# Kernel tuning notes

Hardware: AMD Instinct MI355X
Metric: run time of the kernel (lower is better)

## Reference

```python
import jax, jax.numpy as jnp
import numpy as np

B, H, W, C = 4, 64, 64, 512
G = 32  # GroupNorm groups
EPS = 1e-6


def setup_inputs() -> dict:
    key = jax.random.key(0)
    ks = jax.random.split(key, 9)
    s = C ** -0.5
    return {
        "x": jax.random.normal(ks[0], (B, H, W, C), dtype=jnp.float32),
        "gn_scale": jnp.ones((C,), dtype=jnp.float32),
        "gn_bias": jnp.zeros((C,), dtype=jnp.float32),
        "wq": jax.random.normal(ks[1], (C, C), dtype=jnp.float32) * s,
        "bq": jnp.zeros((C,), dtype=jnp.float32),
        "wk": jax.random.normal(ks[2], (C, C), dtype=jnp.float32) * s,
        "bk": jnp.zeros((C,), dtype=jnp.float32),
        "wv": jax.random.normal(ks[3], (C, C), dtype=jnp.float32) * s,
        "bv": jnp.zeros((C,), dtype=jnp.float32),
        "wo": jax.random.normal(ks[4], (C, C), dtype=jnp.float32) * s,
        "bo": jnp.zeros((C,), dtype=jnp.float32),
    }


def reference(x, gn_scale, gn_bias, wq, bq, wk, bk, wv, bv, wo, bo):
    b, h, w, c = x.shape
    # GroupNorm(32, eps=1e-6): normalize over (H, W, channels-within-group)
    xg = x.reshape(b, h, w, G, c // G)
    mean = xg.mean(axis=(1, 2, 4), keepdims=True)
    var = xg.var(axis=(1, 2, 4), keepdims=True)
    hn = ((xg - mean) * jax.lax.rsqrt(var + EPS)).reshape(b, h, w, c)
    hn = hn * gn_scale + gn_bias
    # 1x1 convs == per-pixel matmuls
    n = h * w
    hf = hn.reshape(b, n, c)
    q = hf @ wq + bq  # [b, n, c]
    k = hf @ wk + bk
    v = hf @ wv + bv
    # attention with materialized scores (faithful to source math)
    scores = jnp.einsum('bqc,bkc->bqk', q, k) * (c ** -0.5)
    attn = jax.nn.softmax(scores, axis=2)
    o = jnp.einsum('bkc,bqk->bqc', v, attn)  # [b, n, c]
    o = o @ wo + bo
    return o.reshape(b, h, w, c) + x
```

## Files before the change

### kernel.cpp

```cpp
#include <hip/hip_runtime.h>
#include <stdint.h>

typedef unsigned short u16;
typedef __bf16 bf16x8 __attribute__((ext_vector_type(8)));
typedef float f32x4 __attribute__((ext_vector_type(4)));
typedef uint32_t u32x2 __attribute__((ext_vector_type(2)));
typedef uint32_t u32x4 __attribute__((ext_vector_type(4)));

#define NB 4
#define NC 512
#define NG 32
#define NSEQ 4096
#define NM (NB*NSEQ)

#define MFMA_(a,b,c) __builtin_amdgcn_mfma_f32_16x16x32_bf16(a,b,c,0,0,0)
#define SWZ(rl) (((((rl) ^ ((rl)>>2)) & 7)) << 4)

__device__ __forceinline__ u16 f2bf(float f){
  uint32_t u = __builtin_bit_cast(uint32_t, f);
  u += 0x7FFFu + ((u >> 16) & 1u);
  return (u16)(u >> 16);
}
__device__ __forceinline__ float bfu(uint32_t lo16){
  return __builtin_bit_cast(float, lo16 << 16);
}
__device__ __forceinline__ uint32_t pk2(float a, float b){
  return (uint32_t)f2bf(a) | ((uint32_t)f2bf(b) << 16);
}

__device__ __forceinline__ void gll16(const void* g, void* l){
  __builtin_amdgcn_global_load_lds(
      (const __attribute__((address_space(1))) void*)g,
      (__attribute__((address_space(3))) void*)l, 16, 0, 0);
}

__global__ void k_zero(float* p, int n){
  int i = blockIdx.x*blockDim.x + threadIdx.x;
  if (i < n) p[i] = 0.f;
}

__global__ __launch_bounds__(256) void k_gn_stats(const float* __restrict__ x, float* __restrict__ stats){
  int blk = blockIdx.x;
  int ch = blk & 7, bg = blk >> 3;
  int g = bg & (NG-1), b = bg >> 5;
  int t = threadIdx.x;
  const float* base = x + (size_t)b*NSEQ*NC + g*16 + (t&3)*4;
  float s1 = 0.f, s2 = 0.f;
  for (int p = ch*512 + (t>>2); p < (ch+1)*512; p += 64){
    float4 v = *(const float4*)(base + (size_t)p*NC);
    s1 += v.x+v.y+v.z+v.w;
    s2 += v.x*v.x + v.y*v.y + v.z*v.z + v.w*v.w;
  }
  #pragma unroll
  for (int o = 32; o; o >>= 1){ s1 += __shfl_xor(s1, o); s2 += __shfl_xor(s2, o); }
  __shared__ float a1[4], a2[4];
  if ((t & 63) == 0){ a1[t>>6] = s1; a2[t>>6] = s2; }
  __syncthreads();
  if (t == 0){
    atomicAdd(&stats[bg*2+0], a1[0]+a1[1]+a1[2]+a1[3]);
    atomicAdd(&stats[bg*2+1], a2[0]+a2[1]+a2[2]+a2[3]);
  }
}

__global__ __launch_bounds__(256) void k_gn_apply(const float* __restrict__ x, const float* __restrict__ stats,
    const float* __restrict__ gsc, const float* __restrict__ gbi, u16* __restrict__ hn){
  const float inv_cnt = 1.f/((float)NSEQ*16.f);
  size_t total = (size_t)NM*NC/4;
  for (size_t i = (size_t)blockIdx.x*blockDim.x + threadIdx.x; i < total; i += (size_t)gridDim.x*blockDim.x){
    size_t flat = i*4;
    int c = (int)(flat & (NC-1));
    int b = (int)(flat >> 21);
    int g = c >> 4;
    float s1 = stats[(b*NG+g)*2], s2 = stats[(b*NG+g)*2+1];
    float mean = s1*inv_cnt;
    float rstd = rsqrtf(s2*inv_cnt - mean*mean + 1e-6f);
    float4 v = *(const float4*)(x + flat);
    float4 sc = *(const float4*)(gsc + c);
    float4 bi = *(const float4*)(gbi + c);
    ushort4 o;
    o.x = f2bf((v.x-mean)*rstd*sc.x + bi.x);
    o.y = f2bf((v.y-mean)*rstd*sc.y + bi.y);
    o.z = f2bf((v.z-mean)*rstd*sc.z + bi.z);
    o.w = f2bf((v.w-mean)*rstd*sc.w + bi.w);
    *(ushort4*)(hn + flat) = o;
  }
}

__global__ __launch_bounds__(256) void k_wtrans4(const float* __restrict__ wq, const float* __restrict__ wk,
    const float* __restrict__ wv, const float* __restrict__ wo,
    u16* __restrict__ wqkvT, u16* __restrict__ woT){
  int j = blockIdx.x*256 + threadIdx.x;
  int wsel = j >> 18, r = j & 262143;
  int n = r >> 9, k = r & 511;
  const float* src = wsel==0?wq : wsel==1?wk : wsel==2?wv : wo;
  u16 v = f2bf(src[k*512 + n]);
  if (wsel < 3) wqkvT[(size_t)wsel*262144 + r] = v;
  else          woT[r] = v;
}

__global__ __launch_bounds__(256) void k_sumred(const float* __restrict__ part, float* __restrict__ sums){
  int row = blockIdx.x*4 + (threadIdx.x >> 6);
  int l = threadIdx.x & 63;
  float s = part[(size_t)row*64 + l];
  #pragma unroll
  for (int o = 32; o; o >>= 1) s += __shfl_xor(s, o);
  if (l == 0) sums[row] = s;
}

__global__ __launch_bounds__(256) void k_pvred(const u16* __restrict__ op, const float* __restrict__ sums,
    u16* __restrict__ o){
  size_t i = ((size_t)blockIdx.x*256 + threadIdx.x)*8;
  int row = (int)(i >> 9);
  float inv = 1.f/sums[row];
  u32x4 a = __builtin_nontemporal_load((const u32x4*)(op + i));
  u32x4 b = __builtin_nontemporal_load((const u32x4*)(op + (size_t)NM*NC + i));
  uint32_t r[4];
  #pragma unroll
  for (int j=0;j<4;j++){
    float lo = (bfu(a[j] & 0xFFFFu) + bfu(b[j] & 0xFFFFu)) * inv;
    float hi = (__builtin_bit_cast(float, a[j] & 0xFFFF0000u) +
                __builtin_bit_cast(float, b[j] & 0xFFFF0000u)) * inv;
    r[j] = (uint32_t)f2bf(lo) | ((uint32_t)f2bf(hi) << 16);
  }
  *(uint4*)(o + i) = make_uint4(r[0], r[1], r[2], r[3]);
}

#define PH_A  { __builtin_amdgcn_sched_barrier(0); __builtin_amdgcn_s_barrier(); \
  asm volatile("s_waitcnt lgkmcnt(0)" ::: "memory"); __builtin_amdgcn_sched_barrier(0); \
  __builtin_amdgcn_s_setprio(1); }
#define PH_B  { __builtin_amdgcn_s_setprio(0); __builtin_amdgcn_sched_barrier(0); \
  __builtin_amdgcn_s_barrier(); }
#define PH_BV { __builtin_amdgcn_s_setprio(0); __builtin_amdgcn_sched_barrier(0); \
  asm volatile("s_waitcnt vmcnt(8)" ::: "memory"); __builtin_amdgcn_s_barrier(); }

template<int MODE>
__global__ __launch_bounds__(512, 2) void k_gemm8(
    const u16* __restrict__ A, const u16* __restrict__ B,
    size_t aBatch, size_t bBatch, int lda_, int ldb_, int Klen, float alpha,
    void* __restrict__ out0,
    const float* __restrict__ aux1)
{
  __shared__ u16 LDS[65536];
  const size_t lda = lda_, ldb = ldb_;
  const int t = threadIdx.x;
  const int l = t & 63, w = t >> 6;
  const int wr = w >> 2, wc = w & 3;
  const int frow = l & 15, kq = l >> 4;
  const int nx = gridDim.x, ny = gridDim.y;
  int f = ((int)blockIdx.z*ny + (int)blockIdx.y)*nx + (int)blockIdx.x;
  const int nwg = nx*ny*(int)gridDim.z;
  f = (f & 7)*(nwg >> 3) + (f >> 3);
  const int bx = f % nx; const int t2 = f / nx;
  const int by = t2 % ny; const int bz = t2 / ny;
  int bb = 0, kOff = 0;
  if constexpr (MODE == 4){ bb = bz & 3; kOff = (bz >> 2)*(NSEQ/2); }
  const int brow = by*256, bcol = bx*256;

  f32x4 acc[8][4] = {};
  const int kswz = 8*(((t&7) ^ (t>>3) ^ (t>>5)) & 7);
  const u16* Ast = A + (size_t)bb*aBatch + (size_t)(brow + (t>>3))*lda + kOff + kswz;
  const u16* Bst = B + (size_t)bb*bBatch + (size_t)(bcol + (t>>3))*ldb + kOff + kswz;
  char* Lb = (char*)LDS;
  char* stD = Lb + t*16;

  auto stage = [&](int buf, int isB, int half, int kt){
    const u16* s = (isB ? Bst : Ast) + (size_t)(half*128)*(isB?ldb:lda) + (size_t)kt*64;
    char* d = stD + buf*65536 + isB*32768 + half*16384;
    gll16(s, d);
    gll16(s + (size_t)64*(isB?ldb:lda), d + 8192);
  };
  auto ldA = [&](int buf, int quad, bf16x8* dst){
    const char* base = Lb + buf*65536 + wr*16384;
    #pragma unroll
    for (int mf=0; mf<4; mf++)
      #pragma unroll
      for (int ks=0; ks<2; ks++){
        int rl = quad*64 + mf*16 + frow;
        int byte = (rl*128 + ks*64 + kq*16) ^ SWZ(rl);
        dst[mf*2+ks] = *(const bf16x8*)(base + byte);
      }
  };
  auto ldB = [&](int buf, int qc, bf16x8* dst){
    const char* base = Lb + buf*65536 + 32768 + (wc>>1)*16384;
    #pragma unroll
    for (int nf=0; nf<2; nf++)
      #pragma unroll
      for (int ks=0; ks<2; ks++){
        int rl = (wc&1)*64 + 4*frow + qc*2 + nf;
        int byte = (rl*128 + ks*64 + kq*16) ^ SWZ(rl);
        dst[nf*2+ks] = *(const bf16x8*)(base + byte);
      }
  };
  auto quad = [&](int qr, int qc, const bf16x8* af, const bf16x8* bf){
    #pragma unroll
    for (int mf=0; mf<4; mf++)
      #pragma unroll
      for (int nf=0; nf<2; nf++)
        #pragma unroll
        for (int ks=0; ks<2; ks++)
          acc[qr*4+mf][qc*2+nf] = MFMA_(af[mf*2+ks], bf[nf*2+ks], acc[qr*4+mf][qc*2+nf]);
  };

  bf16x8 af[8], b0[4], b1[4];
  const int NT = Klen >> 6;
  stage(0,0,0,0); stage(0,0,1,0); stage(0,1,0,0); stage(0,1,1,0);
  stage(1,0,0,1); stage(1,0,1,1); stage(1,1,0,1); stage(1,1,1,1);
  asm volatile("s_waitcnt vmcnt(8)" ::: "memory");
  __builtin_amdgcn_s_barrier();

  for (int i = 0; i < (NT>>1); i++){
    const int st0 = (2*i+2 < NT) ? 2*i+2 : NT-1;
    const int st1 = (2*i+3 < NT) ? 2*i+3 : NT-1;
    ldA(0,0,af); ldB(0,0,b0);
    PH_A; quad(0,0,af,b0); PH_B;
    ldB(0,1,b1);
    PH_A; quad(0,1,af,b1); PH_B;
    ldA(0,1,af);
    stage(0,1,0,st0); stage(0,1,1,st0);
    PH_A; quad(1,0,af,b0); PH_B;
    stage(0,0,0,st0); stage(0,0,1,st0);
    PH_A; quad(1,1,af,b1); PH_BV;
    ldA(1,0,af); ldB(1,0,b0);
    PH_A; quad(0,0,af,b0); PH_B;
    ldB(1,1,b1);
    PH_A; quad(0,1,af,b1); PH_B;
    ldA(1,1,af);
    stage(1,1,0,st1); stage(1,1,1,st1);
    PH_A; quad(1,0,af,b0); PH_B;
    stage(1,0,0,st1); stage(1,0,1,st1);
    PH_A; quad(1,1,af,b1); PH_BV;
  }

  const int col4 = wc*64 + 4*frow;
  if constexpr (MODE==4){
    const int sp = bz >> 2;
    u16* op = (u16*)out0 + (size_t)sp*NM*NC + (size_t)bb*NSEQ*NC;
    #pragma unroll
    for (int m=0;m<8;m++){
      #pragma unroll
      for (int r=0;r<4;r++){
        const int rr = brow + wr*128 + m*16 + kq*4 + r;
        u32x2 wv;
        wv[0] = pk2(acc[m][0][r], acc[m][1][r]);
        wv[1] = pk2(acc[m][2][r], acc[m][3][r]);
        __builtin_nontemporal_store(wv, (u32x2*)&op[(size_t)rr*NC + bcol + col4]);
      }
    }
  }
}

#define NTQ 16

__device__ __forceinline__ int dec_rl(int L, int p){ return 2*L + ((p>>2) ^ ((L>>1)&1)); }
__device__ __forceinline__ int dec_kq(int L, int p){
  int P01 = ((((L)&1)^((L>>2)&1))<<1) | (((L>>1)&1)^((L>>3)&1));
  return (p&3) ^ P01;
}
__device__ __forceinline__ int swz_off(int rl, int kq){
  int Pq = (((rl&1)^((rl>>2)&1))<<2) | ((((rl>>1)&1)^((rl>>3)&1))<<1) | (((rl>>2)&1)^((rl>>4)&1));
  return ((rl>>1)<<7) + ((Pq ^ kq)<<4);
}

template<int MODE>
__global__ __launch_bounds__(512, 4) void k_t512(
    const u16* __restrict__ A, const u16* __restrict__ B,
    void* __restrict__ out0, void* __restrict__ out1, void* __restrict__ out2,
    float* __restrict__ partsum,
    const float* __restrict__ bias0, const float* __restrict__ bias1, const float* __restrict__ bias2,
    float alpha)
{
  __shared__ u16 LDS[36864];
  char* Lb = (char*)LDS;
  const int t = threadIdx.x;
  const int l = t & 63, w = t >> 6;
  const int wr = w >> 2, wc = w & 3;
  const int frow = l & 15, kq = l >> 4;
  const int nx = gridDim.x, ny = gridDim.y;
  int f = ((int)blockIdx.z*ny + (int)blockIdx.y)*nx + (int)blockIdx.x;
  const int nwg = nx*ny*(int)gridDim.z;
  f = (f & 7)*(nwg >> 3) + (f >> 3);
  const int bx = f % nx; const int t2 = f / nx;
  const int by = t2 % ny; const int bb = t2 / ny;
  const int brow = by*128, bcol = bx*256;
  const size_t batchOff = (MODE==1) ? (size_t)bb*NSEQ*NC : 0;

  const int pA = t & 7;
  const int LA = t >> 3;
  const int LB0 = t >> 3, LB1 = 64 + (t >> 3);
  const int rlA  = dec_rl(LA, pA),  kqA  = dec_kq(LA, pA);
  const int rlB0 = dec_rl(LB0, pA), kqB0 = dec_kq(LB0, pA);
  const int rlB1 = dec_rl(LB1, pA), kqB1 = dec_kq(LB1, pA);
  const u16* Ap  = A + batchOff + (size_t)(brow + rlA )*NC + kqA*8;
  const u16* Bp0 = B + batchOff + (size_t)(bcol + rlB0)*NC + kqB0*8;
  const u16* Bp1 = B + batchOff + (size_t)(bcol + rlB1)*NC + kqB1*8;

  auto stage = [&](int buf, int kt){
    const size_t ko = (size_t)kt*32;
    gll16(Bp0 + ko, Lb + buf*16384 + t*16);
    gll16(Bp1 + ko, Lb + buf*16384 + 8192 + t*16);
    gll16(Ap  + ko, Lb + 49152 + buf*8192 + t*16);
  };

  int offA[4], offB[4];
  #pragma unroll
  for (int m=0;m<4;m++) offA[m] = swz_off(wr*64 + m*16 + frow, kq);
  #pragma unroll
  for (int c=0;c<4;c++) offB[c] = swz_off(wc*64 + 4*frow + c, kq);

  f32x4 acc[4][4] = {};

  auto body = [&](int buf, int s){
    bf16x8 a4[4], b4[4];
    #pragma unroll
    for (int m=0;m<4;m++) a4[m] = *(const bf16x8*)(Lb + 49152 + buf*8192 + offA[m]);
    #pragma unroll
    for (int c=0;c<4;c++) b4[c] = *(const bf16x8*)(Lb + buf*16384 + offB[c]);
    const bool doStage = (s + 2 < NTQ);
    if (doStage){ int nb = buf+2; if (nb>=3) nb-=3; stage(nb, s+2); }
    asm volatile("s_waitcnt lgkmcnt(0)" ::: "memory");
    __builtin_amdgcn_sched_barrier(0);
    __builtin_amdgcn_s_setprio(1);
    #pragma unroll
    for (int m=0;m<4;m++)
      #pragma unroll
      for (int c=0;c<4;c++)
        acc[m][c] = MFMA_(a4[m], b4[c], acc[m][c]);
    __builtin_amdgcn_s_setprio(0);
    __builtin_amdgcn_sched_barrier(0);
    if (s + 1 < NTQ){
      if (doStage) asm volatile("s_waitcnt vmcnt(3)" ::: "memory");
      else         asm volatile("s_waitcnt vmcnt(0)" ::: "memory");
      __builtin_amdgcn_s_barrier();
    }
  };

  stage(0, 0); stage(1, 1);
  asm volatile("s_waitcnt vmcnt(3)" ::: "memory");
  __builtin_amdgcn_s_barrier();

  #pragma unroll
  for (int i = 0; i < 5; i++){
    body(0, i*3);
    body(1, i*3+1);
    body(2, i*3+2);
  }
  body(0, 15);

  const int col4 = wc*64 + 4*frow;
  if constexpr (MODE==0){
    const int seg = bcol >> 9;
    const int colr = (bcol & 511) + col4;
    if (seg < 2){
      u16* dq = (u16*)(seg==0 ? out0 : out1);
      const float* bp = seg==0 ? bias0 : bias1;
      const float4 bi = *(const float4*)(bp + colr);
      #pragma unroll
      for (int m=0;m<4;m++){
        #pragma unroll
        for (int r=0;r<4;r++){
          const int rr = brow + wr*64 + m*16 + kq*4 + r;
          u32x2 wv;
          wv[0] = pk2(acc[m][0][r]+bi.x, acc[m][1][r]+bi.y);
          wv[1] = pk2(acc[m][2][r]+bi.z, acc[m][3][r]+bi.w);
          *(u32x2*)&dq[(size_t)rr*NC + colr] = wv;
        }
      }
    } else {
      const float4 bi = *(const float4*)(bias2 + colr);
      const float bvs[4] = {bi.x, bi.y, bi.z, bi.w};
      #pragma unroll
      for (int m=0;m<4;m++){
        const int rr0 = brow + wr*64 + m*16 + kq*4;
        const int b = rr0 >> 12, sq = rr0 & 4095;
        #pragma unroll
        for (int n=0;n<4;n++){
          u32x2 wv;
          wv[0] = pk2(acc[m][n][0]+bvs[n], acc[m][n][1]+bvs[n]);
          wv[1] = pk2(acc[m][n][2]+bvs[n], acc[m][n][3]+bvs[n]);
          *(u32x2*)&((u16*)out2)[((size_t)(b*NC + colr + n) << 12) + sq] = wv;
        }
      }
    }
  } else {
    u16* Pp = (u16*)out0 + (size_t)bb*NSEQ*NSEQ;
    const int colg = bcol + col4;
    #pragma unroll
    for (int m=0;m<4;m++){
      #pragma unroll
      for (int r=0;r<4;r++){
        const int rr = brow + wr*64 + m*16 + kq*4 + r;
        float e0 = __expf(alpha*acc[m][0][r]);
        float e1 = __expf(alpha*acc[m][1][r]);
        float e2 = __expf(alpha*acc[m][2][r]);
        float e3 = __expf(alpha*acc[m][3][r]);
        u32x2 wv; wv[0] = pk2(e0, e1); wv[1] = pk2(e2, e3);
        __builtin_nontemporal_store(wv, (u32x2*)&Pp[(size_t)rr*NSEQ + colg]);
        float rs = bfu(wv[0] & 0xFFFFu) + bfu(wv[0] >> 16) + bfu(wv[1] & 0xFFFFu) + bfu(wv[1] >> 16);
        rs += __shfl_xor(rs, 1); rs += __shfl_xor(rs, 2);
        rs += __shfl_xor(rs, 4); rs += __shfl_xor(rs, 8);
        if (frow == 0)
          partsum[((size_t)bb*NSEQ + rr)*64 + bx*4 + wc] = rs;
      }
    }
  }
}

__global__ __launch_bounds__(256, 3) void k_t256o(
    const u16* __restrict__ A, const u16* __restrict__ B,
    float* __restrict__ out, const float* __restrict__ bias, const float* __restrict__ res)
{
  __shared__ u16 LDS[24576];
  char* Lb = (char*)LDS;
  const int t = threadIdx.x;
  const int l = t & 63, w = t >> 6;
  const int wr = w >> 1, wc = w & 1;
  const int frow = l & 15, kq = l >> 4;
  int f = (int)blockIdx.y*4 + (int)blockIdx.x;
  f = (f & 7)*64 + (f >> 3);
  const int bx = f & 3; const int by = f >> 2;
  const int brow = by*128, bcol = bx*128;

  const int pA = t & 7;
  const int L0 = t >> 3;
  const int rl0 = dec_rl(L0, pA),      kq0 = dec_kq(L0, pA);
  const int rl1 = dec_rl(L0+32, pA),   kq1 = dec_kq(L0+32, pA);
  const u16* Ap0 = A + (size_t)(brow + rl0)*NC + kq0*8;
  const u16* Ap1 = A + (size_t)(brow + rl1)*NC + kq1*8;
  const u16* Bp0 = B + (size_t)(bcol + rl0)*NC + kq0*8;
  const u16* Bp1 = B + (size_t)(bcol + rl1)*NC + kq1*8;

  auto stage = [&](int buf, int kt){
    const size_t ko = (size_t)kt*32;
    gll16(Ap0 + ko, Lb + buf*16384 + t*16);
    gll16(Ap1 + ko, Lb + buf*16384 + 4096 + t*16);
    gll16(Bp0 + ko, Lb + buf*16384 + 8192 + t*16);
    gll16(Bp1 + ko, Lb + buf*16384 + 12288 + t*16);
  };

  int offA[4], offB[4];
  #pragma unroll
  for (int m=0;m<4;m++) offA[m] = swz_off(wr*64 + m*16 + frow, kq);
  #pragma unroll
  for (int c=0;c<4;c++) offB[c] = swz_off(wc*64 + 4*frow + c, kq);

  f32x4 acc[4][4] = {};

  auto body = [&](int buf, int s){
    bf16x8 a4[4], b4[4];
    #pragma unroll
    for (int m=0;m<4;m++) a4[m] = *(const bf16x8*)(Lb + buf*16384 + offA[m]);
    #pragma unroll
    for (int c=0;c<4;c++) b4[c] = *(const bf16x8*)(Lb + buf*16384 + 8192 + offB[c]);
    const bool doStage = (s + 2 < NTQ);
    if (doStage){ int nb = buf+2; if (nb>=3) nb-=3; stage(nb, s+2); }
    asm volatile("s_waitcnt lgkmcnt(0)" ::: "memory");
    __builtin_amdgcn_sched_barrier(0);
    __builtin_amdgcn_s_setprio(1);
    #pragma unroll
    for (int m=0;m<4;m++)
      #pragma unroll
      for (int c=0;c<4;c++)
        acc[m][c] = MFMA_(a4[m], b4[c], acc[m][c]);
    __builtin_amdgcn_s_setprio(0);
    __builtin_amdgcn_sched_barrier(0);
    if (s + 1 < NTQ){
      if (doStage) asm volatile("s_waitcnt vmcnt(4)" ::: "memory");
      else         asm volatile("s_waitcnt vmcnt(0)" ::: "memory");
      __builtin_amdgcn_s_barrier();
    }
  };

  stage(0, 0); stage(1, 1);
  asm volatile("s_waitcnt vmcnt(4)" ::: "memory");
  __builtin_amdgcn_s_barrier();

  #pragma unroll
  for (int i = 0; i < 5; i++){
    body(0, i*3);
    body(1, i*3+1);
    body(2, i*3+2);
  }
  body(0, 15);

  const int c = bcol + wc*64 + 4*frow;
  const float4 bi = *(const float4*)(bias + c);
  #pragma unroll
  for (int m=0;m<4;m++){
    #pragma unroll
    for (int r=0;r<4;r++){
      const int rr = brow + wr*64 + m*16 + kq*4 + r;
      const float4 rv = *(const float4*)(res + (size_t)rr*NC + c);
      float4 ov;
      ov.x = acc[m][0][r] + bi.x + rv.x;
      ov.y = acc[m][1][r] + bi.y + rv.y;
      ov.z = acc[m][2][r] + bi.z + rv.z;
      ov.w = acc[m][3][r] + bi.w + rv.w;
      *(float4*)&out[(size_t)rr*NC + c] = ov;
    }
  }
}

extern "C" void kernel_launch(void* const* d_in, const int* in_sizes, int n_in,
                              void* d_out, int out_size, void* d_ws, size_t ws_size,
                              hipStream_t stream){
  const float* x   = (const float*)d_in[0];
  const float* gsc = (const float*)d_in[1];
  const float* gbi = (const float*)d_in[2];
  const float* wq  = (const float*)d_in[3];
  const float* bq  = (const float*)d_in[4];
  const float* wk  = (const float*)d_in[5];
  const float* bk  = (const float*)d_in[6];
  const float* wv  = (const float*)d_in[7];
  const float* bv  = (const float*)d_in[8];
  const float* wo  = (const float*)d_in[9];
  const float* bo  = (const float*)d_in[10];
  float* out = (float*)d_out;

  char* wsp = (char*)d_ws;
  size_t off = 0;
  auto alloc = [&](size_t bytes)->void*{ void* p = wsp + off; off += (bytes + 255) & ~(size_t)255; return p; };
  float* stats   = (float*)alloc((size_t)NB*NG*2*sizeof(float));
  float* sums    = (float*)alloc((size_t)NM*sizeof(float));
  float* partsum = (float*)alloc((size_t)NM*64*sizeof(float));
  u16* hn    = (u16*)alloc((size_t)NM*NC*2);
  u16* wqkvT = (u16*)alloc((size_t)3*NC*NC*2);
  u16* woT   = (u16*)alloc((size_t)NC*NC*2);
  u16* q     = (u16*)alloc((size_t)NM*NC*2);
  u16* kk    = (u16*)alloc((size_t)NM*NC*2);
  u16* vT    = (u16*)alloc((size_t)NM*NC*2);
  u16* o     = (u16*)alloc((size_t)NM*NC*2);
  u16* P     = (u16*)alloc((size_t)NB*NSEQ*NSEQ*2);
  u16* opart = q;

  k_zero<<<1,256,0,stream>>>(stats, NB*NG*2);
  k_gn_stats<<<NB*NG*8,256,0,stream>>>(x, stats);
  k_gn_apply<<<2048,256,0,stream>>>(x, stats, gsc, gbi, hn);
  k_wtrans4<<<4096,256,0,stream>>>(wq, wk, wv, wo, wqkvT, woT);

  k_t512<0><<<dim3(6,128,1),512,0,stream>>>(hn, wqkvT,
      q, kk, vT, nullptr, bq, bk, bv, 1.f);

  const float scale = 0.044194173824159216f;
  k_t512<1><<<dim3(16,32,NB),512,0,stream>>>(q, kk,
      P, nullptr, nullptr, partsum, nullptr, nullptr, nullptr, scale);
  k_sumred<<<NM/4,256,0,stream>>>(partsum, sums);
  k_gemm8<4><<<dim3(2,16,8),512,0,stream>>>(P, vT,
      (size_t)NSEQ*NSEQ, (size_t)NC*NSEQ, NSEQ, NSEQ, NSEQ/2, 1.f,
      opart, nullptr);
  k_pvred<<<NM*NC/8/256,256,0,stream>>>(opart, sums, o);
  k_t256o<<<dim3(4,128,1),256,0,stream>>>(o, woT, out, bo, x);
}
```

Measured before the change: 247.8 us.

## Use FP8 Q/K with FP8 MFMA for scores and restructure GroupNorm passes

The QKV projection now writes Q and K as FP8 (e4m3 via cvt_pk_fp8) and a new QK^T kernel uses the fp8 16x16x32 MFMA with a triple-buffered LDS pipeline. This halves Q/K storage and traffic and raises matrix throughput for the score GEMM. GroupNorm stats now also write a bf16 copy of x, so the apply pass reads half the bytes. The risks are FP8 precision loss in the attention scores, scalar uncoalesced 2-byte P stores in the new epilogue, and an extra bf16 rounding of x before normalization.

```diff
diff --git a/kernel.cpp b/kernel.cpp
--- a/kernel.cpp
+++ b/kernel.cpp
@@ -2,6 +2,7 @@
 #include <stdint.h>
 
 typedef unsigned short u16;
+typedef long i64;
 typedef __bf16 bf16x8 __attribute__((ext_vector_type(8)));
 typedef float f32x4 __attribute__((ext_vector_type(4)));
 typedef uint32_t u32x2 __attribute__((ext_vector_type(2)));
@@ -14,6 +15,7 @@
 #define NM (NB*NSEQ)
 
 #define MFMA_(a,b,c) __builtin_amdgcn_mfma_f32_16x16x32_bf16(a,b,c,0,0,0)
+#define MFMA8_(a,b,c) __builtin_amdgcn_mfma_f32_16x16x32_fp8_fp8(a,b,c,0,0,0)
 #define SWZ(rl) (((((rl) ^ ((rl)>>2)) & 7)) << 4)
 
 __device__ __forceinline__ u16 f2bf(float f){
@@ -39,51 +41,64 @@
   if (i < n) p[i] = 0.f;
 }
 
-__global__ __launch_bounds__(256) void k_gn_stats(const float* __restrict__ x, float* __restrict__ stats){
+__global__ __launch_bounds__(256) void k_gn_stats2(const float* __restrict__ x,
+    u16* __restrict__ xbf, float* __restrict__ stats){
   int blk = blockIdx.x;
-  int ch = blk & 7, bg = blk >> 3;
-  int g = bg & (NG-1), b = bg >> 5;
+  int b = blk >> 6, ch = blk & 63;
   int t = threadIdx.x;
-  const float* base = x + (size_t)b*NSEQ*NC + g*16 + (t&3)*4;
+  int colv = t & 127;
+  int r0 = ch*64 + (t >> 7);
+  const float* xp = x  + (size_t)b*NSEQ*NC + (size_t)r0*NC + colv*4;
+  u16* xb       = xbf + (size_t)b*NSEQ*NC + (size_t)r0*NC + colv*4;
   float s1 = 0.f, s2 = 0.f;
-  for (int p = ch*512 + (t>>2); p < (ch+1)*512; p += 64){
-    float4 v = *(const float4*)(base + (size_t)p*NC);
+  #pragma unroll 4
+  for (int i = 0; i < 32; i++){
+    float4 v = *(const float4*)(xp + (size_t)i*2*NC);
     s1 += v.x+v.y+v.z+v.w;
-    s2 += v.x*v.x + v.y*v.y + v.z*v.z + v.w*v.w;
-  }
-  #pragma unroll
-  for (int o = 32; o; o >>= 1){ s1 += __shfl_xor(s1, o); s2 += __shfl_xor(s2, o); }
-  __shared__ float a1[4], a2[4];
-  if ((t & 63) == 0){ a1[t>>6] = s1; a2[t>>6] = s2; }
+    s2 += v.x*v.x+v.y*v.y+v.z*v.z+v.w*v.w;
+    ushort4 o; o.x=f2bf(v.x); o.y=f2bf(v.y); o.z=f2bf(v.z); o.w=f2bf(v.w);
+    *(ushort4*)(xb + (size_t)i*2*NC) = o;
+  }
+  s1 += __shfl_xor(s1,1); s2 += __shfl_xor(s2,1);
+  s1 += __shfl_xor(s1,2); s2 += __shfl_xor(s2,2);
+  __shared__ float ls1[4][16], ls2[4][16];
+  int w = t >> 6, l = t & 63;
+  if ((l & 3) == 0){ ls1[w][l>>2] = s1; ls2[w][l>>2] = s2; }
   __syncthreads();
-  if (t == 0){
-    atomicAdd(&stats[bg*2+0], a1[0]+a1[1]+a1[2]+a1[3]);
-    atomicAdd(&stats[bg*2+1], a2[0]+a2[1]+a2[2]+a2[3]);
-  }
-}
-
-__global__ __launch_bounds__(256) void k_gn_apply(const float* __restrict__ x, const float* __restrict__ stats,
-    const float* __restrict__ gsc, const float* __restrict__ gbi, u16* __restrict__ hn){
+  if (t < 32){
+    int g = t;
+    int wlo = g >> 4;
+    float a1 = ls1[wlo][g&15] + ls1[wlo+2][g&15];
+    float a2 = ls2[wlo][g&15] + ls2[wlo+2][g&15];
+    atomicAdd(&stats[(b*NG+g)*2+0], a1);
+    atomicAdd(&stats[(b*NG+g)*2+1], a2);
+  }
+}
+
+__global__ __launch_bounds__(256) void k_gn_apply2(const u16* __restrict__ xbf,
+    const float* __restrict__ stats, const float* __restrict__ gsc,
+    const float* __restrict__ gbi, u16* __restrict__ hn){
   const float inv_cnt = 1.f/((float)NSEQ*16.f);
-  size_t total = (size_t)NM*NC/4;
-  for (size_t i = (size_t)blockIdx.x*blockDim.x + threadIdx.x; i < total; i += (size_t)gridDim.x*blockDim.x){
-    size_t flat = i*4;
-    int c = (int)(flat & (NC-1));
-    int b = (int)(flat >> 21);
-    int g = c >> 4;
-    float s1 = stats[(b*NG+g)*2], s2 = stats[(b*NG+g)*2+1];
-    float mean = s1*inv_cnt;
-    float rstd = rsqrtf(s2*inv_cnt - mean*mean + 1e-6f);
-    float4 v = *(const float4*)(x + flat);
-    float4 sc = *(const float4*)(gsc + c);
-    float4 bi = *(const float4*)(gbi + c);
-    ushort4 o;
-    o.x = f2bf((v.x-mean)*rstd*sc.x + bi.x);
-    o.y = f2bf((v.y-mean)*rstd*sc.y + bi.y);
-    o.z = f2bf((v.z-mean)*rstd*sc.z + bi.z);
-    o.w = f2bf((v.w-mean)*rstd*sc.w + bi.w);
-    *(ushort4*)(hn + flat) = o;
-  }
+  size_t i = ((size_t)blockIdx.x*256 + threadIdx.x)*8;
+  int c = (int)(i & 511);
+  int b = (int)(i >> 21);
+  int g = c >> 4;
+  float s1 = stats[(b*NG+g)*2], s2 = stats[(b*NG+g)*2+1];
+  float mean = s1*inv_cnt;
+  float rstd = rsqrtf(s2*inv_cnt - mean*mean + 1e-6f);
+  u32x4 v = *(const u32x4*)(xbf + i);
+  float4 scA = *(const float4*)(gsc + c), scB = *(const float4*)(gsc + c + 4);
+  float4 biA = *(const float4*)(gbi + c), biB = *(const float4*)(gbi + c + 4);
+  const float sc[8] = {scA.x,scA.y,scA.z,scA.w,scB.x,scB.y,scB.z,scB.w};
+  const float bi[8] = {biA.x,biA.y,biA.z,biA.w,biB.x,biB.y,biB.z,biB.w};
+  u32x4 o;
+  #pragma unroll
+  for (int j = 0; j < 4; j++){
+    float lo = bfu(v[j] & 0xFFFFu);
+    float hi = __builtin_bit_cast(float, v[j] & 0xFFFF0000u);
+    o[j] = pk2((lo-mean)*rstd*sc[2*j] + bi[2*j], (hi-mean)*rstd*sc[2*j+1] + bi[2*j+1]);
+  }
+  *(u32x4*)(hn + i) = o;
 }
 
 __global__ __launch_bounds__(256) void k_wtrans4(const float* __restrict__ wq, const float* __restrict__ wk,
@@ -133,12 +148,10 @@
 #define PH_BV { __builtin_amdgcn_s_setprio(0); __builtin_amdgcn_sched_barrier(0); \
   asm volatile("s_waitcnt vmcnt(8)" ::: "memory"); __builtin_amdgcn_s_barrier(); }
 
-template<int MODE>
-__global__ __launch_bounds__(512, 2) void k_gemm8(
+__global__ __launch_bounds__(512, 2) void k_gemm8pv(
     const u16* __restrict__ A, const u16* __restrict__ B,
-    size_t aBatch, size_t bBatch, int lda_, int ldb_, int Klen, float alpha,
-    void* __restrict__ out0,
-    const float* __restrict__ aux1)
+    size_t aBatch, size_t bBatch, int lda_, int ldb_, int Klen,
+    void* __restrict__ out0)
 {
   __shared__ u16 LDS[65536];
   const size_t lda = lda_, ldb = ldb_;
@@ -152,8 +165,7 @@
   f = (f & 7)*(nwg >> 3) + (f >> 3);
   const int bx = f % nx; const int t2 = f / nx;
   const int by = t2 % ny; const int bz = t2 / ny;
-  int bb = 0, kOff = 0;
-  if constexpr (MODE == 4){ bb = bz & 3; kOff = (bz >> 2)*(NSEQ/2); }
+  const int bb = bz & 3, kOff = (bz >> 2)*(NSEQ/2);
   const int brow = by*256, bcol = bx*256;
 
   f32x4 acc[8][4] = {};
@@ -232,19 +244,17 @@
   }
 
   const int col4 = wc*64 + 4*frow;
-  if constexpr (MODE==4){
-    const int sp = bz >> 2;
-    u16* op = (u16*)out0 + (size_t)sp*NM*NC + (size_t)bb*NSEQ*NC;
-    #pragma unroll
-    for (int m=0;m<8;m++){
-      #pragma unroll
-      for (int r=0;r<4;r++){
-        const int rr = brow + wr*128 + m*16 + kq*4 + r;
-        u32x2 wv;
-        wv[0] = pk2(acc[m][0][r], acc[m][1][r]);
-        wv[1] = pk2(acc[m][2][r], acc[m][3][r]);
-        __builtin_nontemporal_store(wv, (u32x2*)&op[(size_t)rr*NC + bcol + col4]);
-      }
+  const int sp = bz >> 2;
+  u16* op = (u16*)out0 + (size_t)sp*NM*NC + (size_t)bb*NSEQ*NC;
+  #pragma unroll
+  for (int m=0;m<8;m++){
+    #pragma unroll
+    for (int r=0;r<4;r++){
+      const int rr = brow + wr*128 + m*16 + kq*4 + r;
+      u32x2 wv;
+      wv[0] = pk2(acc[m][0][r], acc[m][1][r]);
+      wv[1] = pk2(acc[m][2][r], acc[m][3][r]);
+      __builtin_nontemporal_store(wv, (u32x2*)&op[(size_t)rr*NC + bcol + col4]);
     }
   }
 }
@@ -261,13 +271,10 @@
   return ((rl>>1)<<7) + ((Pq ^ kq)<<4);
 }
 
-template<int MODE>
-__global__ __launch_bounds__(512, 4) void k_t512(
+__global__ __launch_bounds__(512, 4) void k_qkv(
     const u16* __restrict__ A, const u16* __restrict__ B,
-    void* __restrict__ out0, void* __restrict__ out1, void* __restrict__ out2,
-    float* __restrict__ partsum,
-    const float* __restrict__ bias0, const float* __restrict__ bias1, const float* __restrict__ bias2,
-    float alpha)
+    uint8_t* __restrict__ q8, uint8_t* __restrict__ k8, u16* __restrict__ vT,
+    const float* __restrict__ bias0, const float* __restrict__ bias1, const float* __restrict__ bias2)
 {
   __shared__ u16 LDS[36864];
   char* Lb = (char*)LDS;
@@ -276,13 +283,11 @@
   const int wr = w >> 2, wc = w & 3;
   const int frow = l & 15, kq = l >> 4;
   const int nx = gridDim.x, ny = gridDim.y;
-  int f = ((int)blockIdx.z*ny + (int)blockIdx.y)*nx + (int)blockIdx.x;
-  const int nwg = nx*ny*(int)gridDim.z;
+  int f = (int)blockIdx.y*nx + (int)blockIdx.x;
+  const int nwg = nx*ny;
   f = (f & 7)*(nwg >> 3) + (f >> 3);
-  const int bx = f % nx; const int t2 = f / nx;
-  const int by = t2 % ny; const int bb = t2 / ny;
+  const int bx = f % nx; const int by = f / nx;
   const int brow = by*128, bcol = bx*256;
-  const size_t batchOff = (MODE==1) ? (size_t)bb*NSEQ*NC : 0;
 
   const int pA = t & 7;
   const int LA = t >> 3;
@@ -290,9 +295,9 @@
   const int rlA  = dec_rl(LA, pA),  kqA  = dec_kq(LA, pA);
   const int rlB0 = dec_rl(LB0, pA), kqB0 = dec_kq(LB0, pA);
   const int rlB1 = dec_rl(LB1, pA), kqB1 = dec_kq(LB1, pA);
-  const u16* Ap  = A + batchOff + (size_t)(brow + rlA )*NC + kqA*8;
-  const u16* Bp0 = B + batchOff + (size_t)(bcol + rlB0)*NC + kqB0*8;
-  const u16* Bp1 = B + batchOff + (size_t)(bcol + rlB1)*NC + kqB1*8;
+  const u16* Ap  = A + (size_t)(brow + rlA )*NC + kqA*8;
+  const u16* Bp0 = B + (size_t)(bcol + rlB0)*NC + kqB0*8;
+  const u16* Bp1 = B + (size_t)(bcol + rlB1)*NC + kqB1*8;
 
   auto stage = [&](int buf, int kt){
     const size_t ko = (size_t)kt*32;
@@ -347,60 +352,140 @@
   body(0, 15);
 
   const int col4 = wc*64 + 4*frow;
-  if constexpr (MODE==0){
-    const int seg = bcol >> 9;
-    const int colr = (bcol & 511) + col4;
-    if (seg < 2){
-      u16* dq = (u16*)(seg==0 ? out0 : out1);
-      const float* bp = seg==0 ? bias0 : bias1;
-      const float4 bi = *(const float4*)(bp + colr);
-      #pragma unroll
-      for (int m=0;m<4;m++){
-        #pragma unroll
-        for (int r=0;r<4;r++){
-          const int rr = brow + wr*64 + m*16 + kq*4 + r;
-          u32x2 wv;
-          wv[0] = pk2(acc[m][0][r]+bi.x, acc[m][1][r]+bi.y);
-          wv[1] = pk2(acc[m][2][r]+bi.z, acc[m][3][r]+bi.w);
-          *(u32x2*)&dq[(size_t)rr*NC + colr] = wv;
-        }
-      }
-    } else {
-      const float4 bi = *(const float4*)(bias2 + colr);
-      const float bvs[4] = {bi.x, bi.y, bi.z, bi.w};
-      #pragma unroll
-      for (int m=0;m<4;m++){
-        const int rr0 = brow + wr*64 + m*16 + kq*4;
-        const int b = rr0 >> 12, sq = rr0 & 4095;
-        #pragma unroll
-        for (int n=0;n<4;n++){
-          u32x2 wv;
-          wv[0] = pk2(acc[m][n][0]+bvs[n], acc[m][n][1]+bvs[n]);
-          wv[1] = pk2(acc[m][n][2]+bvs[n], acc[m][n][3]+bvs[n]);
-          *(u32x2*)&((u16*)out2)[((size_t)(b*NC + colr + n) << 12) + sq] = wv;
-        }
-      }
-    }
-  } else {
-    u16* Pp = (u16*)out0 + (size_t)bb*NSEQ*NSEQ;
-    const int colg = bcol + col4;
+  const int seg = bcol >> 9;
+  const int colr = (bcol & 511) + col4;
+  if (seg < 2){
+    uint8_t* dq = seg==0 ? q8 : k8;
+    const float* bp = seg==0 ? bias0 : bias1;
+    const float4 bi = *(const float4*)(bp + colr);
     #pragma unroll
     for (int m=0;m<4;m++){
       #pragma unroll
       for (int r=0;r<4;r++){
         const int rr = brow + wr*64 + m*16 + kq*4 + r;
-        float e0 = __expf(alpha*acc[m][0][r]);
-        float e1 = __expf(alpha*acc[m][1][r]);
-        float e2 = __expf(alpha*acc[m][2][r]);
-        float e3 = __expf(alpha*acc[m][3][r]);
-        u32x2 wv; wv[0] = pk2(e0, e1); wv[1] = pk2(e2, e3);
-        __builtin_nontemporal_store(wv, (u32x2*)&Pp[(size_t)rr*NSEQ + colg]);
-        float rs = bfu(wv[0] & 0xFFFFu) + bfu(wv[0] >> 16) + bfu(wv[1] & 0xFFFFu) + bfu(wv[1] >> 16);
-        rs += __shfl_xor(rs, 1); rs += __shfl_xor(rs, 2);
-        rs += __shfl_xor(rs, 4); rs += __shfl_xor(rs, 8);
-        if (frow == 0)
-          partsum[((size_t)bb*NSEQ + rr)*64 + bx*4 + wc] = rs;
+        unsigned int pv = __builtin_amdgcn_cvt_pk_fp8_f32(acc[m][0][r]+bi.x, acc[m][1][r]+bi.y, 0u, false);
+        pv = __builtin_amdgcn_cvt_pk_fp8_f32(acc[m][2][r]+bi.z, acc[m][3][r]+bi.w, pv, true);
+        *(unsigned int*)&dq[(size_t)rr*NC + colr] = pv;
       }
+    }
+  } else {
+    const float4 bi = *(const float4*)(bias2 + colr);
+    const float bvs[4] = {bi.x, bi.y, bi.z, bi.w};
+    #pragma unroll
+    for (int m=0;m<4;m++){
+      const int rr0 = brow + wr*64 + m*16 + kq*4;
+      const int b = rr0 >> 12, sq = rr0 & 4095;
+      #pragma unroll
+      for (int n=0;n<4;n++){
+        u32x2 wv;
+        wv[0] = pk2(acc[m][n][0]+bvs[n], acc[m][n][1]+bvs[n]);
+        wv[1] = pk2(acc[m][n][2]+bvs[n], acc[m][n][3]+bvs[n]);
+        *(u32x2*)&vT[((size_t)(b*NC + colr + n) << 12) + sq] = wv;
+      }
+    }
+  }
+}
+
+__global__ __launch_bounds__(512, 4) void k_qk8(
+    const uint8_t* __restrict__ Q8, const uint8_t* __restrict__ K8,
+    u16* __restrict__ P, float* __restrict__ partsum, float alpha)
+{
+  __shared__ char LDS[73728];
+  char* LA = LDS;
+  char* LB = LDS + 24576;
+  const int t = threadIdx.x;
+  const int l = t & 63, w = t >> 6;
+  const int wr = w >> 2, wc = w & 3;
+  const int frow = l & 15, kq = l >> 4;
+  int f = ((int)blockIdx.z*32 + (int)blockIdx.y)*16 + (int)blockIdx.x;
+  f = (f & 7)*256 + (f >> 3);
+  const int bx = f & 15; const int t2 = f >> 4;
+  const int by = t2 & 31; const int bb = t2 >> 5;
+  const int brow = by*128, bcol = bx*256;
+  const size_t bOff = (size_t)bb*NSEQ*NC;
+
+  auto srcoff = [](int u)->int{
+    int Lp = u>>3, p2 = u&7;
+    int rl = 2*Lp + (p2>>2);
+    int gr = (p2&3) ^ (Lp&3);
+    return rl*NC + gr*16;
+  };
+  const uint8_t* Ap  = Q8 + bOff + (size_t)brow*NC + srcoff(t);
+  const uint8_t* Bp0 = K8 + bOff + (size_t)bcol*NC + srcoff(t);
+  const uint8_t* Bp1 = K8 + bOff + (size_t)bcol*NC + srcoff(t + 512);
+
+  auto stage = [&](int buf, int kt){
+    const size_t ko = (size_t)kt*64;
+    gll16(Ap  + ko, LA + buf*8192 + t*16);
+    gll16(Bp0 + ko, LB + buf*16384 + t*16);
+    gll16(Bp1 + ko, LB + buf*16384 + 8192 + t*16);
+  };
+
+  auto rdoff = [](int rl, int ks)->int{
+    int slot8 = ((rl&1)<<3) | (((((ks>>1) ^ (rl>>1)) & 3))<<1) | (ks&1);
+    return ((rl>>1)<<7) + (slot8<<3);
+  };
+  int offA[4], offB[4];
+  #pragma unroll
+  for (int m=0;m<4;m++) offA[m] = rdoff(wr*64 + m*16 + frow, kq);
+  #pragma unroll
+  for (int n=0;n<4;n++) offB[n] = rdoff(wc*64 + n*16 + frow, kq);
+
+  f32x4 acc[4][4] = {};
+
+  auto body = [&](int buf, int s){
+    i64 a0[4], a1[4], b0[4], b1[4];
+    const char* Ab = LA + buf*8192;
+    const char* Bb = LB + buf*16384;
+    #pragma unroll
+    for (int m=0;m<4;m++){ a0[m] = *(const i64*)(Ab + offA[m]); a1[m] = *(const i64*)(Ab + (offA[m]^32)); }
+    #pragma unroll
+    for (int n=0;n<4;n++){ b0[n] = *(const i64*)(Bb + offB[n]); b1[n] = *(const i64*)(Bb + (offB[n]^32)); }
+    const bool doStage = (s + 2 < 8);
+    if (doStage){ int nb = buf+2; if (nb>=3) nb-=3; stage(nb, s+2); }
+    asm volatile("s_waitcnt lgkmcnt(0)" ::: "memory");
+    __builtin_amdgcn_sched_barrier(0);
+    __builtin_amdgcn_s_setprio(1);
+    #pragma unroll
+    for (int m=0;m<4;m++)
+      #pragma unroll
+      for (int n=0;n<4;n++){
+        acc[m][n] = MFMA8_(a0[m], b0[n], acc[m][n]);
+        acc[m][n] = MFMA8_(a1[m], b1[n], acc[m][n]);
+      }
+    __builtin_amdgcn_s_setprio(0);
+    __builtin_amdgcn_sched_barrier(0);
+    if (s + 1 < 8){
+      if (doStage) asm volatile("s_waitcnt vmcnt(3)" ::: "memory");
+      else         asm volatile("s_waitcnt vmcnt(0)" ::: "memory");
+      __builtin_amdgcn_s_barrier();
+    }
+  };
+
+  stage(0, 0); stage(1, 1);
+  asm volatile("s_waitcnt vmcnt(3)" ::: "memory");
+  __builtin_amdgcn_s_barrier();
+
+  body(0,0); body(1,1); body(2,2); body(0,3);
+  body(1,4); body(2,5); body(0,6); body(1,7);
+
+  u16* Pp = P + (size_t)bb*NSEQ*NSEQ;
+  #pragma unroll
+  for (int m=0;m<4;m++){
+    #pragma unroll
+    for (int r=0;r<4;r++){
+      const int rr = brow + wr*64 + m*16 + kq*4 + r;
+      float rs = 0.f;
+      #pragma unroll
+      for (int n=0;n<4;n++){
+        u16 pv = f2bf(__expf(alpha*acc[m][n][r]));
+        Pp[(size_t)rr*NSEQ + bcol + wc*64 + n*16 + frow] = pv;
+        rs += bfu(pv);
+      }
+      rs += __shfl_xor(rs, 1); rs += __shfl_xor(rs, 2);
+      rs += __shfl_xor(rs, 4); rs += __shfl_xor(rs, 8);
+      if (frow == 0)
+        partsum[((size_t)bb*NSEQ + rr)*64 + bx*4 + wc] = rs;
     }
   }
 }
@@ -522,31 +607,29 @@
   float* stats   = (float*)alloc((size_t)NB*NG*2*sizeof(float));
   float* sums    = (float*)alloc((size_t)NM*sizeof(float));
   float* partsum = (float*)alloc((size_t)NM*64*sizeof(float));
+  u16* xbf   = (u16*)alloc((size_t)NM*NC*2);
   u16* hn    = (u16*)alloc((size_t)NM*NC*2);
   u16* wqkvT = (u16*)alloc((size_t)3*NC*NC*2);
   u16* woT   = (u16*)alloc((size_t)NC*NC*2);
-  u16* q     = (u16*)alloc((size_t)NM*NC*2);
-  u16* kk    = (u16*)alloc((size_t)NM*NC*2);
+  uint8_t* q8 = (uint8_t*)alloc((size_t)NM*NC);
+  uint8_t* k8 = (uint8_t*)alloc((size_t)NM*NC);
   u16* vT    = (u16*)alloc((size_t)NM*NC*2);
   u16* o     = (u16*)alloc((size_t)NM*NC*2);
   u16* P     = (u16*)alloc((size_t)NB*NSEQ*NSEQ*2);
-  u16* opart = q;
+  u16* opart = xbf;
 
   k_zero<<<1,256,0,stream>>>(stats, NB*NG*2);
-  k_gn_stats<<<NB*NG*8,256,0,stream>>>(x, stats);
-  k_gn_apply<<<2048,256,0,stream>>>(x, stats, gsc, gbi, hn);
+  k_gn_stats2<<<NB*64,256,0,stream>>>(x, xbf, stats);
+  k_gn_apply2<<<4096,256,0,stream>>>(xbf, stats, gsc, gbi, hn);
   k_wtrans4<<<4096,256,0,stream>>>(wq, wk, wv, wo, wqkvT, woT);
 
-  k_t512<0><<<dim3(6,128,1),512,0,stream>>>(hn, wqkvT,
-      q, kk, vT, nullptr, bq, bk, bv, 1.f);
+  k_qkv<<<dim3(6,128,1),512,0,stream>>>(hn, wqkvT, q8, k8, vT, bq, bk, bv);
 
   const float scale = 0.044194173824159216f;
-  k_t512<1><<<dim3(16,32,NB),512,0,stream>>>(q, kk,
-      P, nullptr, nullptr, partsum, nullptr, nullptr, nullptr, scale);
+  k_qk8<<<dim3(16,32,NB),512,0,stream>>>(q8, k8, P, partsum, scale);
   k_sumred<<<NM/4,256,0,stream>>>(partsum, sums);
-  k_gemm8<4><<<dim3(2,16,8),512,0,stream>>>(P, vT,
-      (size_t)NSEQ*NSEQ, (size_t)NC*NSEQ, NSEQ, NSEQ, NSEQ/2, 1.f,
-      opart, nullptr);
+  k_gemm8pv<<<dim3(2,16,8),512,0,stream>>>(P, vT,
+      (size_t)NSEQ*NSEQ, (size_t)NC*NSEQ, NSEQ, NSEQ, NSEQ/2, opart);
   k_pvred<<<NM*NC/8/256,256,0,stream>>>(opart, sums, o);
   k_t256o<<<dim3(4,128,1),256,0,stream>>>(o, woT, out, bo, x);
 }
```

Result: faster. 229.2 us (-7.5%).
